# Performance work log

Hardware: AMD Instinct MI355X
Metric: run time of the kernel (lower is better)

Reference implementation:

```python
import jax, jax.numpy as jnp
import numpy as np

RC = 6.0          # cutoff radius (init kwarg rc)
K_RADIAL = 8      # radial basis max power
LMAX = 2          # max Legendre degree (hardcoded P0,P1,P2 as in source)
N_RAD_ANG = 3     # angular radial powers n = 0..2


def _cosine_cutoff(r, rc):
    x = jnp.clip(r / rc, 0.0, 1.0)
    return 0.5 * (jnp.cos(jnp.pi * x) + 1.0)


def setup_inputs() -> dict:
    key = jax.random.key(0)
    kR, kZ = jax.random.split(key)
    N = 192
    L = 20.0  # cubic box edge, Angstrom
    R = jax.random.uniform(kR, (N, 3), dtype=jnp.float32) * L
    Z = jax.random.randint(kZ, (N,), 0, 4, dtype=jnp.int32)
    box = (jnp.eye(3, dtype=jnp.float32) * L)
    return {"R": R, "Z": Z, "box": box}


def reference(R, Z, box):
    # R: [N,3], Z: [N] (unused, kept for extensibility), box: [3,3]
    N = R.shape[0]
    dtype = R.dtype

    # --- minimum-image pairwise displacements: dr[i,j] = R[i] - R[j] (MIC) ---
    box_inv = jnp.linalg.inv(box)
    s = jnp.einsum('ij,nj->ni', box_inv, R)              # fractional coords [N,3]
    ds = s[:, None, :] - s[None, :, :]                   # [N,N,3]
    ds = ds - jnp.round(ds)
    dr = jnp.einsum('ij,nmj->nmi', box, ds)              # [N,N,3]
    rij = jnp.linalg.norm(dr + 1e-16, axis=-1)           # [N,N]

    fc = _cosine_cutoff(rij, RC)                         # [N,N]
    mask = 1.0 - jnp.eye(N, dtype=dtype)                 # exclude self (i==j)
    fcm = fc * mask                                      # [N,N]

    # --- radial descriptor: q_r[i,k] = sum_j rij^k * fc(rij), k=0..K ---
    powers = jnp.arange(K_RADIAL + 1)
    Phi = rij[..., None] ** powers                       # [N,N,K+1]
    q_r = jnp.sum(Phi * fcm[..., None], axis=1)          # [N,K+1]

    # --- angular descriptor (3-body) ---
    dot = jnp.einsum('ijc,ikc->ijk', dr, dr)             # [N,N,N]
    cos = jnp.clip(dot / (rij[:, :, None] * rij[:, None, :] + 1e-8), -1.0, 1.0)
    # Legendre P0,P1,P2
    P = jnp.stack([jnp.ones_like(cos), cos, 0.5 * (3.0 * cos**2 - 1.0)], axis=-1)  # [N,N,N,3]
    rprod = rij[:, :, None] * rij[:, None, :]            # rij*rik, [N,N,N]
    r_terms = rprod[..., None] ** jnp.arange(N_RAD_ANG)  # (rij*rik)^n, [N,N,N,3]
    fc_pair = fcm[:, :, None] * fcm[:, None, :]          # cutoff + pair mask folded in, [N,N,N]
    feat = fc_pair[..., None, None] * r_terms[..., None] * P[..., None, :]  # [N,N,N,3,3]
    q_ang = jnp.sum(feat, axis=(1, 2)).reshape(N, -1)    # [N, n_rad*(Lmax+1)] = [N,9]

    return jnp.concatenate([q_r, q_ang], axis=-1)        # [N, 18]
```

## Files before the change

### kernel.cpp

```cpp
#include <hip/hip_runtime.h>
#include <math.h>


namespace {

constexpr float RC_  = 6.0f;
constexpr float PI_F = 3.14159265358979323846f;

__global__ __launch_bounds__(64)
void desc_kernel(const float* __restrict__ R,
                 const float* __restrict__ box,
                 float* __restrict__ out,
                 int N)
{
    const int i    = blockIdx.x;
    const int lane = threadIdx.x;

    const float b00 = box[0], b01 = box[1], b02 = box[2];
    const float b10 = box[3], b11 = box[4], b12 = box[5];
    const float b20 = box[6], b21 = box[7], b22 = box[8];
    const float c00 =  (b11 * b22 - b12 * b21);
    const float c10 = -(b10 * b22 - b12 * b20);
    const float c20 =  (b10 * b21 - b11 * b20);
    const float det = b00 * c00 + b01 * c10 + b02 * c20;
    const float id  = 1.0f / det;
    const float i00 = c00 * id;
    const float i01 = (b02 * b21 - b01 * b22) * id;
    const float i02 = (b01 * b12 - b02 * b11) * id;
    const float i10 = c10 * id;
    const float i11 = (b00 * b22 - b02 * b20) * id;
    const float i12 = (b02 * b10 - b00 * b12) * id;
    const float i20 = c20 * id;
    const float i21 = (b01 * b20 - b00 * b21) * id;
    const float i22 = (b00 * b11 - b01 * b10) * id;

    const float Rix = R[3 * i + 0], Riy = R[3 * i + 1], Riz = R[3 * i + 2];
    const float six = i00 * Rix + i01 * Riy + i02 * Riz;
    const float siy = i10 * Rix + i11 *Riy + i12 * Riz;
    const float siz = i20 * Rix + i21 * Riy + i22 * Riz;

    float qr[9];
#pragma unroll
    for (int k = 0; k < 9; ++k) qr[k] = 0.0f;
    float V[3][3];
    float M[3][6];
#pragma unroll
    for (int n = 0; n < 3; ++n) {
#pragma unroll
        for (int c = 0; c < 3; ++c) V[n][c] = 0.0f;
#pragma unroll
        for (int c = 0; c < 6; ++c) M[n][c] = 0.0f;
    }

    for (int j = lane; j < N; j += 64) {
        if (j == i) continue;
        const float Rjx = R[3 * j + 0], Rjy = R[3 * j + 1], Rjz = R[3 * j + 2];
        const float sjx = i00 * Rjx + i01 * Rjy + i02 * Rjz;
        const float sjy = i10 * Rjx + i11 * Rjy + i12 * Rjz;
        const float sjz = i20 * Rjx + i21 * Rjy + i22 * Rjz;
        float dsx = six - sjx; dsx -= rintf(dsx);
        float dsy = siy - sjy; dsy -= rintf(dsy);
        float dsz = siz - sjz; dsz -= rintf(dsz);
        const float dx = b00 * dsx + b01 * dsy + b02 * dsz;
        const float dy = b10 * dsx + b11 * dsy + b12 * dsz;
        const float dz = b20 * dsx + b21 * dsy + b22 * dsz;
        const float r2 = dx * dx + dy * dy + dz * dz;
        const float r  = sqrtf(r2);
        if (r >= RC_) continue;

        const float fc = 0.5f * (__cosf(PI_F * (r * (1.0f / RC_))) + 1.0f);

        float rp = 1.0f;
#pragma unroll
        for (int k = 0; k < 9; ++k) { qr[k] += rp * fc; rp *= r; }

        const float ir = 1.0f / r;
        const float ux = dx * ir, uy = dy * ir, uz = dz * ir;
        float w = fc;
#pragma unroll
        for (int n = 0; n < 3; ++n) {
            V[n][0] += w * ux;      V[n][1] += w * uy;      V[n][2] += w * uz;
            M[n][0] += w * ux * ux; M[n][1] += w * uy * uy; M[n][2] += w * uz * uz;
            M[n][3] += w * ux * uy; M[n][4] += w * ux * uz; M[n][5] += w * uy * uz;
            w *= r;
        }
    }

#pragma unroll
    for (int off = 32; off > 0; off >>= 1) {
#pragma unroll
        for (int k = 0; k < 9; ++k) qr[k] += __shfl_xor(qr[k], off);
#pragma unroll
        for (int n = 0; n < 3; ++n) {
#pragma unroll
            for (int c = 0; c < 3; ++c) V[n][c] += __shfl_xor(V[n][c], off);
#pragma unroll
            for (int c = 0; c < 6; ++c) M[n][c] += __shfl_xor(M[n][c], off);
        }
    }

    if (lane == 0) {
        float* o = out + i * 18;
#pragma unroll
        for (int k = 0; k < 9; ++k) o[k] = qr[k];
#pragma unroll
        for (int n = 0; n < 3; ++n) {
            const float s  = qr[n];
            const float v2 = V[n][0] * V[n][0] + V[n][1] * V[n][1] + V[n][2] * V[n][2];
            const float m2 = M[n][0] * M[n][0] + M[n][1] * M[n][1] + M[n][2] * M[n][2]
                     + 2.0f * (M[n][3] * M[n][3] + M[n][4] * M[n][4] + M[n][5] * M[n][5]);
            o[9 + n * 3 + 0] = s * s;
            o[9 + n * 3 + 1] = v2;
            o[9 + n * 3 + 2] = 1.5f * m2 - 0.5f * s * s;
        }
    }
}

}

extern "C" void kernel_launch(void* const* d_in, const int* in_sizes, int n_in,
                              void* d_out, int out_size, void* d_ws, size_t ws_size,
                              hipStream_t stream)
{
    const float* R   = (const float*)d_in[0];
    const float* box = (const float*)d_in[2];
    float* out = (float*)d_out;
    const int N = in_sizes[0] / 3;

    desc_kernel<<<dim3(N), dim3(64), 0, stream>>>(R, box, out, N);
}
```

Baseline: 60.09 us.

## Branchless pair accumulation, DPP wave reductions, and N=192 specialized path

Rewrites the per-pair body to be branchless: it masks invalid pairs with a select, compares r² against the squared cutoff, builds radial powers from squares, and uses a hardware reciprocal. It drops one quadrupole accumulator by recovering Mzz from the trace identity. It replaces the shfl_xor butterfly with DPP- and swizzle-based reductions and adds a fully unrolled path for N=192 that preloads all positions. Outputs are written as float2. The aim is to cut divergence, instruction count and cross-lane reduction latency in a tiny, latency-bound kernel.

```diff
diff --git a/kernel.cpp b/kernel.cpp
--- a/kernel.cpp
+++ b/kernel.cpp
@@ -5,7 +5,84 @@
 namespace {
 
 constexpr float RC_  = 6.0f;
+constexpr float RC2_ = RC_ * RC_;
 constexpr float PI_F = 3.14159265358979323846f;
+
+struct Ctx {
+    float b00, b01, b02, b10, b11, b12, b20, b21, b22;
+    float i00, i01, i02, i10, i11, i12, i20, i21, i22;
+    float six, siy, siz;
+    int   i;
+};
+
+template<int CTRL>
+__device__ __forceinline__ float dpp_add(float v) {
+    int t = __builtin_amdgcn_update_dpp(0, __builtin_bit_cast(int, v),
+                                        CTRL, 0xF, 0xF, true);
+    return v + __builtin_bit_cast(float, t);
+}
+
+__device__ __forceinline__ float wave_allreduce(float v) {
+    v = dpp_add<0xB1>(v);
+    v = dpp_add<0x4E>(v);
+    v = dpp_add<0x141>(v);
+    v = dpp_add<0x140>(v);
+    int t = __builtin_amdgcn_ds_swizzle(__builtin_bit_cast(int, v), 0x401F);
+    v += __builtin_bit_cast(float, t);
+    v += __shfl_xor(v, 32);
+    return v;
+}
+
+__device__ __forceinline__ void pair_accum(const Ctx& c, int j, bool inb,
+                                           float Rjx, float Rjy, float Rjz,
+                                           float qr[9], float V[3][3], float M[3][5])
+{
+    const float sjx = c.i00 * Rjx + c.i01 * Rjy + c.i02 * Rjz;
+    const float sjy = c.i10 * Rjx + c.i11 * Rjy + c.i12 * Rjz;
+    const float sjz = c.i20 * Rjx + c.i21 * Rjy + c.i22 * Rjz;
+    float dsx = c.six - sjx; dsx -= rintf(dsx);
+    float dsy = c.siy - sjy; dsy -= rintf(dsy);
+    float dsz = c.siz - sjz; dsz -= rintf(dsz);
+    const float dx = c.b00 * dsx + c.b01 * dsy + c.b02 * dsz;
+    const float dy = c.b10 * dsx + c.b11 * dsy + c.b12 * dsz;
+    const float dz = c.b20 * dsx + c.b21 * dsy + c.b22 * dsz;
+    const float r2 = dx * dx + dy * dy + dz * dz;
+
+    const bool valid = inb && (j != c.i) && (r2 < RC2_);
+    const float rr = valid ? r2 : 1.0f;
+    const float r  = sqrtf(rr);
+    const float ir = __builtin_amdgcn_rcpf(r);
+    float fc = 0.5f * (__cosf((PI_F / RC_) * r) + 1.0f);
+    fc = valid ? fc : 0.0f;
+
+    const float r3 = rr * r;
+    const float r4 = rr * rr;
+    const float r5 = r4 * r;
+    const float r6 = r3 * r3;
+    const float r7 = r3 * r4;
+    const float r8 = r4 * r4;
+    qr[0] += fc;
+    qr[1] += fc * r;
+    qr[2] += fc * rr;
+    qr[3] += fc * r3;
+    qr[4] += fc * r4;
+    qr[5] += fc * r5;
+    qr[6] += fc * r6;
+    qr[7] += fc * r7;
+    qr[8] += fc * r8;
+
+    const float h1 = fc * ir;
+    const float h0 = h1 * ir;
+    const float g2 = fc * r;
+    V[0][0] += h1 * dx; V[0][1] += h1 * dy; V[0][2] += h1 * dz;
+    V[1][0] += fc * dx; V[1][1] += fc * dy; V[1][2] += fc * dz;
+    V[2][0] += g2 * dx; V[2][1] += g2 * dy; V[2][2] += g2 * dz;
+    const float dxx = dx * dx, dyy = dy * dy;
+    const float dxy = dx * dy, dxz = dx * dz, dyz = dy * dz;
+    M[0][0] += h0 * dxx; M[0][1] += h0 * dyy; M[0][2] += h0 * dxy; M[0][3] += h0 * dxz; M[0][4] += h0 * dyz;
+    M[1][0] += h1 * dxx; M[1][1] += h1 * dyy; M[1][2] += h1 * dxy; M[1][3] += h1 * dxz; M[1][4] += h1 * dyz;
+    M[2][0] += fc * dxx; M[2][1] += fc * dyy; M[2][2] += fc * dxy; M[2][3] += fc * dxz; M[2][4] += fc * dyz;
+}
 
 __global__ __launch_bounds__(64)
 void desc_kernel(const float* __restrict__ R,
@@ -16,103 +93,97 @@
     const int i    = blockIdx.x;
     const int lane = threadIdx.x;
 
-    const float b00 = box[0], b01 = box[1], b02 = box[2];
-    const float b10 = box[3], b11 = box[4], b12 = box[5];
-    const float b20 = box[6], b21 = box[7], b22 = box[8];
-    const float c00 =  (b11 * b22 - b12 * b21);
-    const float c10 = -(b10 * b22 - b12 * b20);
-    const float c20 =  (b10 * b21 - b11 * b20);
-    const float det = b00 * c00 + b01 * c10 + b02 * c20;
+    Ctx c;
+    c.i = i;
+    c.b00 = box[0]; c.b01 = box[1]; c.b02 = box[2];
+    c.b10 = box[3]; c.b11 = box[4]; c.b12 = box[5];
+    c.b20 = box[6]; c.b21 = box[7]; c.b22 = box[8];
+    const float c00 =  (c.b11 * c.b22 - c.b12 * c.b21);
+    const float c10 = -(c.b10 * c.b22 - c.b12 * c.b20);
+    const float c20 =  (c.b10 * c.b21 - c.b11 * c.b20);
+    const float det = c.b00 * c00 + c.b01 * c10 + c.b02 * c20;
     const float id  = 1.0f / det;
-    const float i00 = c00 * id;
-    const float i01 = (b02 * b21 - b01 * b22) * id;
-    const float i02 = (b01 * b12 - b02 * b11) * id;
-    const float i10 = c10 * id;
-    const float i11 = (b00 * b22 - b02 * b20) * id;
-    const float i12 = (b02 * b10 - b00 * b12) * id;
-    const float i20 = c20 * id;
-    const float i21 = (b01 * b20 - b00 * b21) * id;
-    const float i22 = (b00 * b11 - b01 * b10) * id;
+    c.i00 = c00 * id;
+    c.i01 = (c.b02 * c.b21 - c.b01 * c.b22) * id;
+    c.i02 = (c.b01 * c.b12 - c.b02 * c.b11) * id;
+    c.i10 = c10 * id;
+    c.i11 = (c.b00 * c.b22 - c.b02 * c.b20) * id;
+    c.i12 = (c.b02 * c.b10 - c.b00 * c.b12) * id;
+    c.i20 = c20 * id;
+    c.i21 = (c.b01 * c.b20 - c.b00 * c.b21) * id;
+    c.i22 = (c.b00 * c.b11 - c.b01 * c.b10) * id;
 
     const float Rix = R[3 * i + 0], Riy = R[3 * i + 1], Riz = R[3 * i + 2];
-    const float six = i00 * Rix + i01 * Riy + i02 * Riz;
-    const float siy = i10 * Rix + i11 *Riy + i12 * Riz;
-    const float siz = i20 * Rix + i21 * Riy + i22 * Riz;
+    c.six = c.i00 * Rix + c.i01 * Riy + c.i02 * Riz;
+    c.siy = c.i10 * Rix + c.i11 * Riy + c.i12 * Riz;
+    c.siz = c.i20 * Rix + c.i21 * Riy + c.i22 * Riz;
 
     float qr[9];
+    float V[3][3];
+    float M[3][5];
 #pragma unroll
     for (int k = 0; k < 9; ++k) qr[k] = 0.0f;
-    float V[3][3];
-    float M[3][6];
 #pragma unroll
     for (int n = 0; n < 3; ++n) {
 #pragma unroll
-        for (int c = 0; c < 3; ++c) V[n][c] = 0.0f;
-#pragma unroll
-        for (int c = 0; c < 6; ++c) M[n][c] = 0.0f;
-    }
-
-    for (int j = lane; j < N; j += 64) {
-        if (j == i) continue;
-        const float Rjx = R[3 * j + 0], Rjy = R[3 * j + 1], Rjz = R[3 * j + 2];
-        const float sjx = i00 * Rjx + i01 * Rjy + i02 * Rjz;
-        const float sjy = i10 * Rjx + i11 * Rjy + i12 * Rjz;
-        const float sjz = i20 * Rjx + i21 * Rjy + i22 * Rjz;
-        float dsx = six - sjx; dsx -= rintf(dsx);
-        float dsy = siy - sjy; dsy -= rintf(dsy);
-        float dsz = siz - sjz; dsz -= rintf(dsz);
-        const float dx = b00 * dsx + b01 * dsy + b02 * dsz;
-        const float dy = b10 * dsx + b11 * dsy + b12 * dsz;
-        const float dz = b20 * dsx + b21 * dsy + b22 * dsz;
-        const float r2 = dx * dx + dy * dy + dz * dz;
-        const float r  = sqrtf(r2);
-        if (r >= RC_) continue;
-
-        const float fc = 0.5f * (__cosf(PI_F * (r * (1.0f / RC_))) + 1.0f);
-
-        float rp = 1.0f;
-#pragma unroll
-        for (int k = 0; k < 9; ++k) { qr[k] += rp * fc; rp *= r; }
-
-        const float ir = 1.0f / r;
-        const float ux = dx * ir, uy = dy * ir, uz = dz * ir;
-        float w = fc;
-#pragma unroll
-        for (int n = 0; n < 3; ++n) {
-            V[n][0] += w * ux;      V[n][1] += w * uy;      V[n][2] += w * uz;
-            M[n][0] += w * ux * ux; M[n][1] += w * uy * uy; M[n][2] += w * uz * uz;
-            M[n][3] += w * ux * uy; M[n][4] += w * ux * uz; M[n][5] += w * uy * uz;
-            w *= r;
+        for (int q = 0; q < 3; ++q) V[n][q] = 0.0f;
+#pragma unroll
+        for (int q = 0; q < 5; ++q) M[n][q] = 0.0f;
+    }
+
+    if (N == 192) {
+        float px[3], py[3], pz[3];
+#pragma unroll
+        for (int t = 0; t < 3; ++t) {
+            const int j = lane + (t << 6);
+            px[t] = R[3 * j + 0];
+            py[t] = R[3 * j + 1];
+            pz[t] = R[3 * j + 2];
         }
-    }
-
-#pragma unroll
-    for (int off = 32; off > 0; off >>= 1) {
-#pragma unroll
-        for (int k = 0; k < 9; ++k) qr[k] += __shfl_xor(qr[k], off);
-#pragma unroll
-        for (int n = 0; n < 3; ++n) {
-#pragma unroll
-            for (int c = 0; c < 3; ++c) V[n][c] += __shfl_xor(V[n][c], off);
-#pragma unroll
-            for (int c = 0; c < 6; ++c) M[n][c] += __shfl_xor(M[n][c], off);
+#pragma unroll
+        for (int t = 0; t < 3; ++t) {
+            const int j = lane + (t << 6);
+            pair_accum(c, j, true, px[t], py[t], pz[t], qr, V, M);
         }
-    }
-
+    } else {
+        for (int j0 = 0; j0 < N; j0 += 64) {
+            const int j  = j0 + lane;
+            const int jc = (j < N) ? j : 0;
+            const float x = R[3 * jc + 0];
+            const float y = R[3 * jc + 1];
+            const float z = R[3 * jc + 2];
+            pair_accum(c, j, j < N, x, y, z, qr, V, M);
+        }
+    }
+
+#pragma unroll
+    for (int k = 0; k < 9; ++k) qr[k] = wave_allreduce(qr[k]);
+#pragma unroll
+    for (int n = 0; n < 3; ++n) {
+#pragma unroll
+        for (int q = 0; q < 3; ++q) V[n][q] = wave_allreduce(V[n][q]);
+#pragma unroll
+        for (int q = 0; q < 5; ++q) M[n][q] = wave_allreduce(M[n][q]);
+    }
+
+    float o[18];
+#pragma unroll
+    for (int k = 0; k < 9; ++k) o[k] = qr[k];
+#pragma unroll
+    for (int n = 0; n < 3; ++n) {
+        const float s   = qr[n];
+        const float mzz = s - M[n][0] - M[n][1];
+        const float v2  = V[n][0] * V[n][0] + V[n][1] * V[n][1] + V[n][2] * V[n][2];
+        const float m2  = M[n][0] * M[n][0] + M[n][1] * M[n][1] + mzz * mzz
+                  + 2.0f * (M[n][2] * M[n][2] + M[n][3] * M[n][3] + M[n][4] * M[n][4]);
+        o[9 + n * 3 + 0] = s * s;
+        o[9 + n * 3 + 1] = v2;
+        o[9 + n * 3 + 2] = 1.5f * m2 - 0.5f * s * s;
+    }
     if (lane == 0) {
-        float* o = out + i * 18;
-#pragma unroll
-        for (int k = 0; k < 9; ++k) o[k] = qr[k];
-#pragma unroll
-        for (int n = 0; n < 3; ++n) {
-            const float s  = qr[n];
-            const float v2 = V[n][0] * V[n][0] + V[n][1] * V[n][1] + V[n][2] * V[n][2];
-            const float m2 = M[n][0] * M[n][0] + M[n][1] * M[n][1] + M[n][2] * M[n][2]
-                     + 2.0f * (M[n][3] * M[n][3] + M[n][4] * M[n][4] + M[n][5] * M[n][5]);
-            o[9 + n * 3 + 0] = s * s;
-            o[9 + n * 3 + 1] = v2;
-            o[9 + n * 3 + 2] = 1.5f * m2 - 0.5f * s * s;
-        }
+        float2* o2 = reinterpret_cast<float2*>(out + i * 18);
+#pragma unroll
+        for (int k = 0; k < 9; ++k) o2[k] = make_float2(o[2 * k + 0], o[2 * k + 1]);
     }
 }
 
```

Measured after the change: 58.22 us. -3.1%, faster.
